# Kernel tuning notes

Measured on AMD Instinct MI355X. Metric: run time of the kernel, lower is better.

The kernel has to match this reference:

```python
import jax, jax.numpy as jnp
import numpy as np

N, D, DOUT = 10000, 128, 128
KS, KN, KC, NCENTER, HID = 32, 16, 16, 3, 32  # HID = D // 4


def setup_inputs() -> dict:
    key = jax.random.key(0)
    ks = jax.random.split(key, 32)
    p = lambda i, shape: jax.random.normal(ks[i], shape, dtype=jnp.float32) * 0.05
    return {
        "ids": jnp.arange(N, dtype=jnp.int64) if jax.config.jax_enable_x64 else jnp.arange(N, dtype=jnp.int32),
        "feats": jax.random.normal(ks[0], (N, D), dtype=jnp.float32),
        "cluster_idx": jax.random.randint(ks[1], (N, NCENTER, KC), 0, N),
        "struct_idx": jax.random.randint(ks[2], (N, KS), 0, N),
        "epo": 100,
        # VertexConv (cluster): Transform convKK grouped conv -> (k,k,D) weight, (k,k) bias; convK1 -> (k,) weight, scalar bias
        "wKK_c": p(3, (KC, KC, D)), "bKK_c": p(4, (KC, KC)), "wK1_c": p(5, (KC,)), "bK1_c": p(6, ()),
        # VertexConv (knn)
        "wKK_n": p(7, (KN, KN, D)), "bKK_n": p(8, (KN, KN)), "wK1_n": p(9, (KN,)), "bK1_n": p(10, ()),
        # VertexConv (structure)
        "wKK_s": p(11, (KS, KS, D)), "bKK_s": p(12, (KS, KS)), "wK1_s": p(13, (KS,)), "bK1_s": p(14, ()),
        # EdgeConv attention MLP: Linear(D, D//4) -> ReLU -> Linear(D//4, 1)
        "ec_w1": p(15, (D, HID)), "ec_b1": p(16, (HID,)), "ec_w2": p(17, (HID,)), "ec_b2": p(18, ()),
        # Final Linear(D, DOUT)
        "fc_w": p(19, (D, DOUT)), "fc_b": p(20, (DOUT,)),
    }


def vertex_conv(x, wKK, bKK, wK1, bK1):
    # x: (N, k, d). Grouped Conv1d(k, k*k, d, groups=k): mult[n,i,j] = <wKK[i,j], x[n,i]> + bKK[i,j]
    mult = jnp.einsum("nid,ijd->nij", x, wKK) + bKK
    mult = jax.nn.softmax(mult, axis=-1)                 # softmax over last dim
    transformed = jnp.einsum("nij,njd->nid", mult, x)    # (N, k, d)
    # Conv1d(k, 1, 1): weighted sum over the k channels
    return jnp.einsum("nkd,k->nd", transformed, wK1) + bK1


def reference(ids, feats, cluster_idx, struct_idx, epo,
              wKK_c, bKK_c, wK1_c, bK1_c,
              wKK_n, bKK_n, wK1_n, bK1_n,
              wKK_s, bKK_s, wK1_s, bK1_s,
              ec_w1, ec_b1, ec_w2, ec_b2, fc_w, fc_b):
    # epo=100 >= all warmups -> all three hyperedge branches active (static).
    # --- cluster hyperedges (precomputed kmeans index table) ---
    c_feats = feats[cluster_idx[ids]]                    # (N, n_center, kc, d)
    hyperedge = [vertex_conv(c_feats[:, c], wKK_c, bKK_c, wK1_c, bK1_c)
                 for c in range(NCENTER)]
    # --- knn hyperedge: cosine similarity + topk (cos_dis) ---
    nrm = jnp.maximum(jnp.linalg.norm(feats, axis=1, keepdims=True), 1e-12)
    xn = feats / nrm
    sim = xn @ xn.T                                      # (N, N) -- memory-dominant
    _, knn_idx = jax.lax.top_k(sim, KN)                  # (N, kn)
    hyperedge.append(vertex_conv(feats[knn_idx[ids]], wKK_n, bKK_n, wK1_n, bK1_n))
    # --- structure hyperedge (precomputed sampled edge_dict table) ---
    hyperedge.append(vertex_conv(feats[struct_idx[ids]], wKK_s, bKK_s, wK1_s, bK1_s))
    x = jnp.stack(hyperedge, axis=1)                     # (N, t, d), t = n_center + 2
    # EdgeConv: MLP attention over the t hyperedges, softmax along t, weighted sum
    h = jax.nn.relu(jnp.einsum("ntd,dh->nth", x, ec_w1) + ec_b1)
    scores = jax.nn.softmax(jnp.einsum("nth,h->nt", h, ec_w2) + ec_b2, axis=1)
    agg = jnp.einsum("nt,ntd->nd", scores, x)            # (N, d)
    # final fc + relu (dropout = identity in eval)
    return jax.nn.relu(agg @ fc_w + fc_b)
```

## Files before the change

### kernel.cpp

```cpp
#include <hip/hip_runtime.h>
#include <cmath>


#define N_NODES 10000
#define D 128
#define DQ 32
#define NCB 3
#define T_HE 5
#define HID_SZ 32
#define NCH 16
#define CHUNK 625
#define TOPK 16
#define TOPM 32

typedef __attribute__((ext_vector_type(8))) short short8;
typedef __attribute__((ext_vector_type(8))) _Float16 half8;
typedef __attribute__((ext_vector_type(4))) float f32x4;
typedef __attribute__((ext_vector_type(16))) float f32x16;

__device__ __forceinline__ unsigned bf16rne(float f) {
  unsigned u = __float_as_uint(f);
  return (u + 0x7FFFu + ((u >> 16) & 1u)) >> 16;
}

__global__ __launch_bounds__(256) void kpre(const float* __restrict__ feats,
                                            const float* __restrict__ wc,
                                            const float* __restrict__ wn,
                                            const float* __restrict__ wstr,
                                            unsigned short* __restrict__ xnh,
                                            _Float16* __restrict__ fH16,
                                            double* __restrict__ normD,
                                            _Float16* __restrict__ wH16) {
  int bx = blockIdx.x;
  int tid = threadIdx.x;
  if (bx < 2500) {
    int n = bx * 4 + (tid >> 6);
    int lane = tid & 63;
    float2 v = ((const float2*)(feats + (size_t)n * D))[lane];
    _Float16 p2[2] = {(_Float16)v.x, (_Float16)v.y};
    ((unsigned*)(fH16 + (size_t)n * D))[lane] = *(const unsigned*)p2;
    double ss = (double)v.x * (double)v.x + (double)v.y * (double)v.y;
#pragma unroll
    for (int o = 32; o > 0; o >>= 1) ss += __shfl_xor(ss, o);
    double nd = fmax(sqrt(ss), 1e-12);
    if (lane == 0) normD[n] = nd;
    float inv = (float)(1.0 / nd);
    ((unsigned*)(xnh + (size_t)n * D))[lane] = bf16rne(v.x * inv) | (bf16rne(v.y * inv) << 16);
  } else {
    int p = (bx - 2500) * 256 + tid;
    if (p >= 98304) return;
    int e = p * 2;
    float2 v;
    if (e < 32768) v = *(const float2*)(wc + e);
    else if (e < 65536) v = *(const float2*)(wn + (e - 32768));
    else v = *(const float2*)(wstr + (e - 65536));
    _Float16 p2[2] = {(_Float16)v.x, (_Float16)v.y};
    ((unsigned*)wH16)[p] = *(const unsigned*)p2;
  }
}

__device__ __forceinline__ void ceu(unsigned& a, unsigned& b) {
  unsigned lo = min(a, b), hi = max(a, b);
  a = lo; b = hi;
}
__device__ __forceinline__ void ceu64(unsigned long long& a, unsigned long long& b) {
  unsigned long long lo = min(a, b), hi = max(a, b);
  a = lo; b = hi;
}
__device__ __forceinline__ void sort16_asc(unsigned (&v)[16]) {
#pragma unroll
  for (int k = 2; k <= 16; k <<= 1) {
#pragma unroll
    for (int j = k >> 1; j > 0; j >>= 1) {
#pragma unroll
      for (int i = 0; i < 16; i++) {
        int x = i ^ j;
        if (x > i) {
          if ((i & k) == 0) ceu(v[i], v[x]);
          else ceu(v[x], v[i]);
        }
      }
    }
  }
}
__device__ __forceinline__ void merge16_asc(unsigned (&run)[16], const unsigned (&b)[16]) {
  unsigned m[16];
#pragma unroll
  for (int i = 0; i < 16; i++) m[i] = max(run[i], b[15 - i]);
#pragma unroll
  for (int j = 8; j > 0; j >>= 1) {
#pragma unroll
    for (int i = 0; i < 16; i++) {
      if ((i & j) == 0) ceu(m[i], m[i + j]);
    }
  }
#pragma unroll
  for (int i = 0; i < 16; i++) run[i] = m[i];
}

__global__ __launch_bounds__(256, 3) void ksim(const unsigned short* __restrict__ xnh,
                                               unsigned* __restrict__ cand) {
  __shared__ short Bb[16 * 128 * 8];
  __shared__ unsigned kb[4][32 * 35];
  int tid = threadIdx.x;
  int w = tid >> 6, lane = tid & 63, l31 = lane & 31, lh = lane >> 5;
  int row0 = blockIdx.x * 128 + w * 32;
  int chunk = blockIdx.y;
  int cbase = chunk * CHUNK;

  short8 afr[8];
  {
    int ar = min(row0 + l31, N_NODES - 1);
    const short8* ap = (const short8*)(xnh + (size_t)ar * D);
#pragma unroll
    for (int ks = 0; ks < 8; ks++) afr[ks] = ap[ks * 2 + lh];
  }

  unsigned run[16];
#pragma unroll
  for (int s = 0; s < 16; s++) run[s] = 0u;
  unsigned* kbw = kb[w];
  int srow = lane >> 1, soff = (lane & 1) * 16;

  for (int ti = 0; ti < 5; ti++) {
    int tb = cbase + ti * 128;
    __syncthreads();
    {
      int ci = tid >> 1, h = tid & 1;
      int gcol = min(tb + ci, N_NODES - 1);
      const short8* gp = (const short8*)(xnh + (size_t)gcol * D);
      short8* bp = (short8*)Bb;
#pragma unroll
      for (int i = 0; i < 8; i++) bp[(h * 8 + i) * 128 + ci] = gp[h * 8 + i];
    }
    __syncthreads();

    f32x16 acc[4];
#pragma unroll
    for (int ni = 0; ni < 4; ni++)
#pragma unroll
      for (int r = 0; r < 16; r++) acc[ni][r] = 0.f;
    const short8* bv = (const short8*)Bb;
#pragma unroll
    for (int ks = 0; ks < 8; ks++) {
      int kp = ks * 2 + lh;
#pragma unroll
      for (int ni = 0; ni < 4; ni++) {
        short8 bf = bv[kp * 128 + ni * 32 + l31];
        acc[ni] = __builtin_amdgcn_mfma_f32_32x32x16_bf16(afr[ks], bf, acc[ni], 0, 0, 0);
      }
    }

#pragma unroll
    for (int ni = 0; ni < 4; ni++) {
      int cb2 = ti * 128 + ni * 32;
#pragma unroll
      for (int reg = 0; reg < 16; reg++) {
        int r = (reg & 3) + 8 * (reg >> 2) + 4 * lh;
        int cic = cb2 + l31;
        unsigned bb = __float_as_uint(acc[ni][reg]);
        unsigned mu = (bb & 0x80000000u) ? ~bb : (bb | 0x80000000u);
        unsigned key = (cic < CHUNK) ? ((mu & 0xFFFFFC00u) | (unsigned)(1023 - cic)) : 0u;
        kbw[r * 35 + l31] = key;
      }
      unsigned bt[16];
      const unsigned* rp = &kbw[srow * 35 + soff];
#pragma unroll
      for (int q = 0; q < 4; q++) {
        uint4 t4 = *(const uint4*)(rp + q * 4);
        bt[q * 4 + 0] = t4.x; bt[q * 4 + 1] = t4.y;
        bt[q * 4 + 2] = t4.z; bt[q * 4 + 3] = t4.w;
      }
      sort16_asc(bt);
      merge16_asc(run, bt);
    }
  }
  {
    unsigned other[16];
#pragma unroll
    for (int s = 0; s < 16; s++) other[s] = (unsigned)__shfl_xor((int)run[s], 1);
    merge16_asc(run, other);
  }
  int grow = row0 + srow;
  if ((lane & 1) == 0 && grow < N_NODES) {
    unsigned* o = cand + ((size_t)grow * NCH + chunk) * 16;
#pragma unroll
    for (int i = 0; i < 16; i += 4)
      *(uint4*)(o + i) = make_uint4(run[i], run[i + 1], run[i + 2], run[i + 3]);
  }
}

__global__ __launch_bounds__(64) void kmerge(const unsigned* __restrict__ cand,
                                             int* __restrict__ candIdx) {
  int row = blockIdx.x * 64 + threadIdx.x;
  if (row >= N_NODES) return;
  unsigned long long run[TOPM];
#pragma unroll
  for (int s = 0; s < TOPM; s++) run[s] = 0ull;
  const uint4* c4 = (const uint4*)(cand + (size_t)row * (NCH * 16));
  for (int ch = 0; ch < NCH; ch++) {
    unsigned b[16];
#pragma unroll
    for (int q = 0; q < 4; q++) {
      uint4 t = c4[ch * 4 + q];
      b[q * 4 + 0] = t.x; b[q * 4 + 1] = t.y;
      b[q * 4 + 2] = t.z; b[q * 4 + 3] = t.w;
    }
    unsigned base = (unsigned)(ch * CHUNK);
    unsigned long long b64[16];
#pragma unroll
    for (int s = 0; s < 16; s++) {
      unsigned k = b[s];
      unsigned gcol = base + (1023u - (k & 1023u));
      b64[s] = ((unsigned long long)(k >> 10) << 32) | (unsigned long long)(~gcol);
    }
#pragma unroll
    for (int i = 0; i < 16; i++) run[i] = max(run[i], b64[15 - i]);
#pragma unroll
    for (int j = 16; j > 0; j >>= 1)
#pragma unroll
      for (int i = 0; i < TOPM; i++)
        if ((i & j) == 0) ceu64(run[i], run[i + j]);
  }
  int4* o4 = (int4*)(candIdx + (size_t)row * TOPM);
#pragma unroll
  for (int s = 0; s < TOPM; s += 4) {
    int4 o;
    o.x = (int)(~(unsigned)(run[s + 0] & 0xFFFFFFFFull));
    o.y = (int)(~(unsigned)(run[s + 1] & 0xFFFFFFFFull));
    o.z = (int)(~(unsigned)(run[s + 2] & 0xFFFFFFFFull));
    o.w = (int)(~(unsigned)(run[s + 3] & 0xFFFFFFFFull));
    o4[s >> 2] = o;
  }
}

__global__ __launch_bounds__(256) void krerank(const float* __restrict__ feats,
                                               const double* __restrict__ normD,
                                               const int* __restrict__ candIdx,
                                               int* __restrict__ knn) {
  __shared__ float rowF[D];
  __shared__ double simL[TOPM];
  __shared__ int idxL[TOPM];
  int row = blockIdx.x;
  int tid = threadIdx.x;
  if (tid < DQ)
    ((float4*)rowF)[tid] = ((const float4*)(feats + (size_t)row * D))[tid];
  int c = tid >> 3, part = tid & 7;
  int cnd = candIdx[(size_t)row * TOPM + c];
  __syncthreads();
  const float4* f4 = (const float4*)(feats + (size_t)cnd * D);
  double acc = 0.0;
#pragma unroll
  for (int g = 0; g < 4; g++) {
    float4 v = f4[part * 4 + g];
    const float* rf = &rowF[(part * 4 + g) * 4];
    acc = fma((double)v.x, (double)rf[0], acc);
    acc = fma((double)v.y, (double)rf[1], acc);
    acc = fma((double)v.z, (double)rf[2], acc);
    acc = fma((double)v.w, (double)rf[3], acc);
  }
  acc += __shfl_down(acc, 4);
  acc += __shfl_down(acc, 2);
  acc += __shfl_down(acc, 1);
  if (part == 0) {
    simL[c] = acc / (normD[row] * normD[cnd]);
    idxL[c] = cnd;
  }
  __syncthreads();
  if (tid < TOPM) {
    double s = simL[tid];
    int idx = idxL[tid];
    int rank = 0;
#pragma unroll
    for (int o = 0; o < TOPM; o++) {
      double so = simL[o];
      int io = idxL[o];
      rank += (so > s || (so == s && io < idx)) ? 1 : 0;
    }
    if (rank < TOPK) knn[(size_t)row * TOPK + rank] = idx;
  }
}

__global__ __launch_bounds__(256) void kvcall(
    const _Float16* __restrict__ fH16,
    const int* __restrict__ cluster_idx, const int* __restrict__ knn,
    const int* __restrict__ struct_idx,
    const _Float16* __restrict__ wH16,
    const float* __restrict__ bKK_c, const float* __restrict__ bKK_n,
    const float* __restrict__ bKK_s,
    const float* __restrict__ wK1_c, const float* __restrict__ bK1_c,
    const float* __restrict__ wK1_n, const float* __restrict__ bK1_n,
    const float* __restrict__ wK1_s, const float* __restrict__ bK1_s,
    float* __restrict__ hx) {
  __shared__ int idxL[16][33];
  __shared__ float coefP[4][16][33];
  __shared__ float coefS[16][33];
  int tid = threadIdx.x;
  int z = blockIdx.y;
  int n0 = blockIdx.x * 16;
  int w = tid >> 6, lane = tid & 63, l15 = lane & 15, quad = lane >> 4;
  const half8* fH = (const half8*)fH16;

  if (z < 4) {
    const int* idxTab; int istr, ioff, woff;
    const float* bKK; const float* wK1; const float* bK1p;
    if (z < 3) { idxTab = cluster_idx; istr = NCB * 16; ioff = z * 16; woff = 0;     bKK = bKK_c; wK1 = wK1_c; bK1p = bK1_c; }
    else       { idxTab = knn;         istr = 16;       ioff = 0;      woff = 32768; bKK = bKK_n; wK1 = wK1_n; bK1p = bK1_n; }
    {
      int nn = tid >> 4, i = tid & 15;
      idxL[nn][i] = idxTab[(size_t)(n0 + nn) * istr + ioff + i];
    }
    __syncthreads();
    const half8* wHv = (const half8*)(wH16 + woff);
    f32x4 coef = {0.f, 0.f, 0.f, 0.f};
#pragma unroll
    for (int ii = 0; ii < 4; ii++) {
      int i = w * 4 + ii;
      int rowi = idxL[l15][i];
      float bkk = bKK[i * 16 + l15];
      f32x4 acc = {0.f, 0.f, 0.f, 0.f};
#pragma unroll
      for (int kc = 0; kc < 4; kc++) {
        half8 ah = fH[(size_t)rowi * 16 + kc * 4 + quad];
        half8 bh = wHv[((size_t)i * 16 + l15) * 16 + kc * 4 + quad];
        acc = __builtin_amdgcn_mfma_f32_16x16x32_f16(ah, bh, acc, 0, 0, 0);
      }
      float wki = wK1[i];
#pragma unroll
      for (int r = 0; r < 4; r++) {
        float v = acc[r] + bkk;
        float mx = v;
#pragma unroll
        for (int msk = 1; msk < 16; msk <<= 1) mx = fmaxf(mx, __shfl_xor(mx, msk));
        float e = __expf(v - mx);
        float s = e;
#pragma unroll
        for (int msk = 1; msk < 16; msk <<= 1) s += __shfl_xor(s, msk);
        coef[r] += wki * (e / s);
      }
    }
#pragma unroll
    for (int r = 0; r < 4; r++) coefP[w][quad * 4 + r][l15] = coef[r];
    __syncthreads();
    {
      int nn = tid >> 4, j = tid & 15;
      coefS[nn][j] = coefP[0][nn][j] + coefP[1][nn][j] + coefP[2][nn][j] + coefP[3][nn][j];
    }
    __syncthreads();
    {
      int nl = tid >> 4, g = tid & 15;
      float bk1 = bK1p[0];
      float a8[8];
#pragma unroll
      for (int t = 0; t < 8; t++) a8[t] = bk1;
      for (int j = 0; j < 16; j++) {
        float cf = coefS[nl][j];
        int rowj = idxL[nl][j];
        half8 xv = fH[(size_t)rowj * 16 + g];
#pragma unroll
        for (int e = 0; e < 8; e++) a8[e] = fmaf(cf, (float)xv[e], a8[e]);
      }
      int node = n0 + nl;
      float4* o = (float4*)(hx + ((size_t)node * T_HE + z) * D + g * 8);
      o[0] = make_float4(a8[0], a8[1], a8[2], a8[3]);
      o[1] = make_float4(a8[4], a8[5], a8[6], a8[7]);
    }
  } else {
    for (int e = tid; e < 512; e += 256) {
      int nn = e >> 5, i = e & 31;
      idxL[nn][i] = struct_idx[(size_t)(n0 + nn) * 32 + i];
    }
    __syncthreads();
    const half8* wHv = (const half8*)(wH16 + 65536);
    f32x4 coef0 = {0.f, 0.f, 0.f, 0.f};
    f32x4 coef1 = {0.f, 0.f, 0.f, 0.f};
#pragma unroll
    for (int ii = 0; ii < 8; ii++) {
      int i = w * 8 + ii;
      int rowi = idxL[l15][i];
      float bk0 = bKK_s[i * 32 + l15];
      float bk1v = bKK_s[i * 32 + 16 + l15];
      f32x4 a0 = {0.f, 0.f, 0.f, 0.f};
      f32x4 a1 = {0.f, 0.f, 0.f, 0.f};
#pragma unroll
      for (int kc = 0; kc < 4; kc++) {
        half8 ah = fH[(size_t)rowi * 16 + kc * 4 + quad];
        half8 b0 = wHv[((size_t)i * 32 + l15) * 16 + kc * 4 + quad];
        half8 b1 = wHv[((size_t)i * 32 + 16 + l15) * 16 + kc * 4 + quad];
        a0 = __builtin_amdgcn_mfma_f32_16x16x32_f16(ah, b0, a0, 0, 0, 0);
        a1 = __builtin_amdgcn_mfma_f32_16x16x32_f16(ah, b1, a1, 0, 0, 0);
      }
      float wki = wK1_s[i];
#pragma unroll
      for (int r = 0; r < 4; r++) {
        float v0 = a0[r] + bk0, v1 = a1[r] + bk1v;
        float mx = fmaxf(v0, v1);
#pragma unroll
        for (int msk = 1; msk < 16; msk <<= 1) mx = fmaxf(mx, __shfl_xor(mx, msk));
        float e0 = __expf(v0 - mx), e1 = __expf(v1 - mx);
        float s = e0 + e1;
#pragma unroll
        for (int msk = 1; msk < 16; msk <<= 1) s += __shfl_xor(s, msk);
        float inv = wki / s;
        coef0[r] += e0 * inv;
        coef1[r] += e1 * inv;
      }
    }
#pragma unroll
    for (int r = 0; r < 4; r++) {
      coefP[w][quad * 4 + r][l15] = coef0[r];
      coefP[w][quad * 4 + r][l15 + 16] = coef1[r];
    }
    __syncthreads();
    for (int e = tid; e < 512; e += 256) {
      int nn = e >> 5, j = e & 31;
      coefS[nn][j] = coefP[0][nn][j] + coefP[1][nn][j] + coefP[2][nn][j] + coefP[3][nn][j];
    }
    __syncthreads();
    {
      int nl = tid >> 4, g = tid & 15;
      float bk1 = bK1_s[0];
      float a8[8];
#pragma unroll
      for (int t = 0; t < 8; t++) a8[t] = bk1;
      for (int j = 0; j < 32; j++) {
        float cf = coefS[nl][j];
        int rowj = idxL[nl][j];
        half8 xv = fH[(size_t)rowj * 16 + g];
#pragma unroll
        for (int e = 0; e < 8; e++) a8[e] = fmaf(cf, (float)xv[e], a8[e]);
      }
      int node = n0 + nl;
      float4* o = (float4*)(hx + ((size_t)node * T_HE + 4) * D + g * 8);
      o[0] = make_float4(a8[0], a8[1], a8[2], a8[3]);
      o[1] = make_float4(a8[4], a8[5], a8[6], a8[7]);
    }
  }
}

__global__ __launch_bounds__(256) void kfinal(const float* __restrict__ hx,
    const float* __restrict__ w1, const float* __restrict__ b1,
    const float* __restrict__ w2, const float* __restrict__ b2p,
    const float* __restrict__ fcw, const float* __restrict__ fcb,
    float* __restrict__ out) {
  __shared__ float xL[8][T_HE][D];
  __shared__ float hL[8][T_HE][HID_SZ];
  __shared__ float scL[8][T_HE];
  __shared__ float aggL[8][D];
  int tid = threadIdx.x;
  int n0 = blockIdx.x * 8;
  const float4* hx4 = (const float4*)hx;
  for (int q = tid; q < 8 * T_HE * DQ; q += 256) {
    int nn = q / (T_HE * DQ);
    int rem = q - nn * (T_HE * DQ);
    int t = rem / DQ;
    int dq = rem & 31;
    int node = n0 + nn;
    float4 val = make_float4(0.f, 0.f, 0.f, 0.f);
    if (node < N_NODES) val = hx4[((size_t)node * T_HE + t) * DQ + dq];
    *(float4*)&xL[nn][t][dq << 2] = val;
  }
  __syncthreads();
  for (int q = tid; q < 8 * T_HE * HID_SZ; q += 256) {
    int nn = q / (T_HE * HID_SZ);
    int rem = q - nn * (T_HE * HID_SZ);
    int t = rem / HID_SZ;
    int hh = rem & (HID_SZ - 1);
    float acc = b1[hh];
    const float4* xv4 = (const float4*)xL[nn][t];
    for (int dq = 0; dq < 32; dq++) {
      float4 xv = xv4[dq];
      int db = dq * 4;
      acc = fmaf(xv.x, w1[(db + 0) * HID_SZ + hh], acc);
      acc = fmaf(xv.y, w1[(db + 1) * HID_SZ + hh], acc);
      acc = fmaf(xv.z, w1[(db + 2) * HID_SZ + hh], acc);
      acc = fmaf(xv.w, w1[(db + 3) * HID_SZ + hh], acc);
    }
    hL[nn][t][hh] = fmaxf(acc, 0.f);
  }
  __syncthreads();
  if (tid < 8 * T_HE) {
    int nn = tid / T_HE, t = tid % T_HE;
    float acc = b2p[0];
    for (int hh = 0; hh < HID_SZ; hh++) acc = fmaf(hL[nn][t][hh], w2[hh], acc);
    scL[nn][t] = acc;
  }
  __syncthreads();
  if (tid < 8) {
    float mx = -1e30f;
#pragma unroll
    for (int t = 0; t < T_HE; t++) mx = fmaxf(mx, scL[tid][t]);
    float e[T_HE];
    float s = 0.f;
#pragma unroll
    for (int t = 0; t < T_HE; t++) { e[t] = expf(scL[tid][t] - mx); s += e[t]; }
    float inv = 1.f / s;
#pragma unroll
    for (int t = 0; t < T_HE; t++) scL[tid][t] = e[t] * inv;
  }
  __syncthreads();
  {
    int nn = tid >> 5, dq = tid & 31;
    float4 acc = make_float4(0.f, 0.f, 0.f, 0.f);
#pragma unroll
    for (int t = 0; t < T_HE; t++) {
      float sw = scL[nn][t];
      float4 xv = *(const float4*)&xL[nn][t][dq << 2];
      acc.x = fmaf(sw, xv.x, acc.x);
      acc.y = fmaf(sw, xv.y, acc.y);
      acc.z = fmaf(sw, xv.z, acc.z);
      acc.w = fmaf(sw, xv.w, acc.w);
    }
    *(float4*)&aggL[nn][dq << 2] = acc;
  }
  __syncthreads();
  {
    int dout = tid & 127, g = tid >> 7;
    float a0 = fcb[dout], a1 = a0, a2 = a0, a3 = a0;
    for (int dq = 0; dq < 32; dq++) {
      int db = dq * 4;
      float wv0 = fcw[(db + 0) * 128 + dout];
      float wv1 = fcw[(db + 1) * 128 + dout];
      float wv2 = fcw[(db + 2) * 128 + dout];
      float wv3 = fcw[(db + 3) * 128 + dout];
      float4 v0 = *(const float4*)&aggL[g * 4 + 0][db];
      float4 v1 = *(const float4*)&aggL[g * 4 + 1][db];
      float4 v2 = *(const float4*)&aggL[g * 4 + 2][db];
      float4 v3 = *(const float4*)&aggL[g * 4 + 3][db];
      a0 = fmaf(v0.x, wv0, fmaf(v0.y, wv1, fmaf(v0.z, wv2, fmaf(v0.w, wv3, a0))));
      a1 = fmaf(v1.x, wv0, fmaf(v1.y, wv1, fmaf(v1.z, wv2, fmaf(v1.w, wv3, a1))));
      a2 = fmaf(v2.x, wv0, fmaf(v2.y, wv1, fmaf(v2.z, wv2, fmaf(v2.w, wv3, a2))));
      a3 = fmaf(v3.x, wv0, fmaf(v3.y, wv1, fmaf(v3.z, wv2, fmaf(v3.w, wv3, a3))));
    }
    int nb = n0 + g * 4;
    if (nb + 0 < N_NODES) out[(size_t)(nb + 0) * 128 + dout] = fmaxf(a0, 0.f);
    if (nb + 1 < N_NODES) out[(size_t)(nb + 1) * 128 + dout] = fmaxf(a1, 0.f);
    if (nb + 2 < N_NODES) out[(size_t)(nb + 2) * 128 + dout] = fmaxf(a2, 0.f);
    if (nb + 3 < N_NODES) out[(size_t)(nb + 3) * 128 + dout] = fmaxf(a3, 0.f);
  }
}

extern "C" void kernel_launch(void* const* d_in, const int* in_sizes, int n_in,
                              void* d_out, int out_size, void* d_ws, size_t ws_size,
                              hipStream_t stream) {
  (void)in_sizes; (void)n_in; (void)out_size; (void)ws_size;
  const float* feats       = (const float*)d_in[1];
  const int*   cluster_idx = (const int*)d_in[2];
  const int*   struct_idx  = (const int*)d_in[3];
  const float* wKK_c = (const float*)d_in[5];
  const float* bKK_c = (const float*)d_in[6];
  const float* wK1_c = (const float*)d_in[7];
  const float* bK1_c = (const float*)d_in[8];
  const float* wKK_n = (const float*)d_in[9];
  const float* bKK_n = (const float*)d_in[10];
  const float* wK1_n = (const float*)d_in[11];
  const float* bK1_n = (const float*)d_in[12];
  const float* wKK_s = (const float*)d_in[13];
  const float* bKK_s = (const float*)d_in[14];
  const float* wK1_s = (const float*)d_in[15];
  const float* bK1_s = (const float*)d_in[16];
  const float* ec_w1 = (const float*)d_in[17];
  const float* ec_b1 = (const float*)d_in[18];
  const float* ec_w2 = (const float*)d_in[19];
  const float* ec_b2 = (const float*)d_in[20];
  const float* fc_w  = (const float*)d_in[21];
  const float* fc_b  = (const float*)d_in[22];
  float* out = (float*)d_out;

  char* wsb = (char*)d_ws;
  unsigned short* xnh = (unsigned short*)(wsb);
  unsigned* cand = (unsigned*)(wsb + 2560000);
  int* candIdx = (int*)(wsb + 12800000);
  double* normD = (double*)(wsb + 14080000);
  _Float16* fH16 = (_Float16*)(wsb + 14160000);
  _Float16* wH16 = (_Float16*)(wsb + 16720000);
  int* knnIdx = (int*)(wsb + 46080000);
  float* hx = (float*)(wsb + 46720000);

  kpre<<<2884, 256, 0, stream>>>(feats, wKK_c, wKK_n, wKK_s,
                                 xnh, fH16, normD, wH16);
  ksim<<<dim3(79, NCH), 256, 0, stream>>>(xnh, cand);
  kmerge<<<(N_NODES + 63) / 64, 64, 0, stream>>>(cand, candIdx);
  krerank<<<N_NODES, 256, 0, stream>>>(feats, normD, candIdx, knnIdx);

  kvcall<<<dim3(625, 5), 256, 0, stream>>>(fH16, cluster_idx, knnIdx, struct_idx,
                                           wH16, bKK_c, bKK_n, bKK_s,
                                           wK1_c, bK1_c, wK1_n, bK1_n, wK1_s, bK1_s, hx);

  kfinal<<<1250, 256, 0, stream>>>(hx, ec_w1, ec_b1, ec_w2, ec_b2, fc_w, fc_b, out);
}
```

Baseline: 390.6 us.

## Swap MFMA operands so each lane holds row results, dropping LDS transpose

The similarity MFMA now takes the column tile as the A operand and the row fragment as B, so the 16 accumulator registers a lane holds belong to a single query row. Each lane can then build its 16 top-k keys directly from registers instead of writing them to a per-wave shared buffer and reading them back transposed. That shared buffer goes away, the final cross-lane merge uses a shuffle across the two half-waves, and only two accumulators are live at a time. Occupancy is raised from 3 to 4 blocks per SIMD to use the freed LDS and registers, which adds register-spill risk.

```diff
diff --git a/kernel.cpp b/kernel.cpp
--- a/kernel.cpp
+++ b/kernel.cpp
@@ -98,10 +98,9 @@
   for (int i = 0; i < 16; i++) run[i] = m[i];
 }
 
-__global__ __launch_bounds__(256, 3) void ksim(const unsigned short* __restrict__ xnh,
+__global__ __launch_bounds__(256, 4) void ksim(const unsigned short* __restrict__ xnh,
                                                unsigned* __restrict__ cand) {
   __shared__ short Bb[16 * 128 * 8];
-  __shared__ unsigned kb[4][32 * 35];
   int tid = threadIdx.x;
   int w = tid >> 6, lane = tid & 63, l31 = lane & 31, lh = lane >> 5;
   int row0 = blockIdx.x * 128 + w * 32;
@@ -119,8 +118,6 @@
   unsigned run[16];
 #pragma unroll
   for (int s = 0; s < 16; s++) run[s] = 0u;
-  unsigned* kbw = kb[w];
-  int srow = lane >> 1, soff = (lane & 1) * 16;
 
   for (int ti = 0; ti < 5; ti++) {
     int tb = cbase + ti * 128;
@@ -135,54 +132,49 @@
     }
     __syncthreads();
 
-    f32x16 acc[4];
-#pragma unroll
-    for (int ni = 0; ni < 4; ni++)
-#pragma unroll
-      for (int r = 0; r < 16; r++) acc[ni][r] = 0.f;
     const short8* bv = (const short8*)Bb;
 #pragma unroll
-    for (int ks = 0; ks < 8; ks++) {
-      int kp = ks * 2 + lh;
-#pragma unroll
-      for (int ni = 0; ni < 4; ni++) {
-        short8 bf = bv[kp * 128 + ni * 32 + l31];
-        acc[ni] = __builtin_amdgcn_mfma_f32_32x32x16_bf16(afr[ks], bf, acc[ni], 0, 0, 0);
-      }
-    }
-
-#pragma unroll
-    for (int ni = 0; ni < 4; ni++) {
-      int cb2 = ti * 128 + ni * 32;
-#pragma unroll
-      for (int reg = 0; reg < 16; reg++) {
-        int r = (reg & 3) + 8 * (reg >> 2) + 4 * lh;
-        int cic = cb2 + l31;
-        unsigned bb = __float_as_uint(acc[ni][reg]);
-        unsigned mu = (bb & 0x80000000u) ? ~bb : (bb | 0x80000000u);
-        unsigned key = (cic < CHUNK) ? ((mu & 0xFFFFFC00u) | (unsigned)(1023 - cic)) : 0u;
-        kbw[r * 35 + l31] = key;
-      }
-      unsigned bt[16];
-      const unsigned* rp = &kbw[srow * 35 + soff];
-#pragma unroll
-      for (int q = 0; q < 4; q++) {
-        uint4 t4 = *(const uint4*)(rp + q * 4);
-        bt[q * 4 + 0] = t4.x; bt[q * 4 + 1] = t4.y;
-        bt[q * 4 + 2] = t4.z; bt[q * 4 + 3] = t4.w;
-      }
-      sort16_asc(bt);
-      merge16_asc(run, bt);
+    for (int half = 0; half < 2; half++) {
+      f32x16 acc[2];
+#pragma unroll
+      for (int nj = 0; nj < 2; nj++)
+#pragma unroll
+        for (int r = 0; r < 16; r++) acc[nj][r] = 0.f;
+#pragma unroll
+      for (int ks = 0; ks < 8; ks++) {
+        int kp = ks * 2 + lh;
+#pragma unroll
+        for (int nj = 0; nj < 2; nj++) {
+          int ni = half * 2 + nj;
+          short8 af = bv[kp * 128 + ni * 32 + l31];
+          acc[nj] = __builtin_amdgcn_mfma_f32_32x32x16_bf16(af, afr[ks], acc[nj], 0, 0, 0);
+        }
+      }
+#pragma unroll
+      for (int nj = 0; nj < 2; nj++) {
+        int ni = half * 2 + nj;
+        unsigned bt[16];
+#pragma unroll
+        for (int reg = 0; reg < 16; reg++) {
+          int m = (reg & 3) + 8 * (reg >> 2) + 4 * lh;
+          int cic = ti * 128 + ni * 32 + m;
+          unsigned bb = __float_as_uint(acc[nj][reg]);
+          unsigned mu = (bb & 0x80000000u) ? ~bb : (bb | 0x80000000u);
+          bt[reg] = (cic < CHUNK) ? ((mu & 0xFFFFFC00u) | (unsigned)(1023 - cic)) : 0u;
+        }
+        sort16_asc(bt);
+        merge16_asc(run, bt);
+      }
     }
   }
   {
     unsigned other[16];
 #pragma unroll
-    for (int s = 0; s < 16; s++) other[s] = (unsigned)__shfl_xor((int)run[s], 1);
+    for (int s = 0; s < 16; s++) other[s] = (unsigned)__shfl_xor((int)run[s], 32);
     merge16_asc(run, other);
   }
-  int grow = row0 + srow;
-  if ((lane & 1) == 0 && grow < N_NODES) {
+  int grow = row0 + l31;
+  if (lh == 0 && grow < N_NODES) {
     unsigned* o = cand + ((size_t)grow * NCH + chunk) * 16;
 #pragma unroll
     for (int i = 0; i < 16; i += 4)
```

Result: faster. 375.7 us (-3.8%).
